# Performance work log

Measured on AMD Instinct MI355X. Metric: run time of the kernel, lower is better.

The kernel has to match this reference:

```python
import jax, jax.numpy as jnp
import numpy as np

N_NODES = 50000
N_EDGES = 1250000
D_FEAT = 64
UNITS = 64


def setup_inputs() -> dict:
    key = jax.random.key(0)
    k1, k2, k3, k4, k5 = jax.random.split(key, 5)
    src = jax.random.normal(k1, (N_NODES, D_FEAT), dtype=jnp.float32)
    edge = jax.random.randint(k2, (N_EDGES,), 0, N_EDGES, dtype=jnp.int32)  # unused by call()
    dst = jax.random.normal(k3, (N_EDGES, D_FEAT), dtype=jnp.float32)
    segment_ids = jnp.sort(
        jax.random.randint(k4, (N_EDGES, 1), 0, N_NODES, dtype=jnp.int32), axis=0
    )
    W = jax.random.normal(k5, (D_FEAT, UNITS), dtype=jnp.float32) * 0.05
    b = jnp.zeros((UNITS,), dtype=jnp.float32)
    return {"src": src, "edge": edge, "dst": dst, "segment_ids": segment_ids, "W": W, "b": b}


def reference(src, edge, dst, segment_ids, W, b):
    # h_i = Dense( segment_mean(dst, ids) + src )
    ids = jnp.squeeze(segment_ids, axis=-1)
    n = src.shape[0]
    sums = jax.ops.segment_sum(dst, ids, num_segments=n, indices_are_sorted=True)  # [N, D]
    counts = jax.ops.segment_sum(
        jnp.ones((ids.shape[0],), dtype=dst.dtype), ids, num_segments=n, indices_are_sorted=True
    )
    # tf.math.segment_mean outputs 0 for empty segments -> guard divide
    mean = sums / jnp.maximum(counts, 1.0)[:, None]  # [N, D]
    x = mean + src  # self-loop residual
    return x @ W + b  # linear activation (activation=None)
```

## Files before the change

### kernel.cpp

```cpp
#include <hip/hip_runtime.h>

constexpr int D = 64;

__global__ void seg_bounds(const int* __restrict__ ids, int* __restrict__ offs,
                           int n_nodes, int n_edges) {
    const int e = blockIdx.x * blockDim.x + threadIdx.x;
    if (e >= n_edges) return;
    const int cur  = ids[e];
    const int prev = (e == 0) ? -1 : ids[e - 1];
    for (int n = prev + 1; n <= cur; ++n) offs[n] = e;
    if (e == n_edges - 1) {
        for (int n = cur + 1; n <= n_nodes; ++n) offs[n] = n_edges;
    }
}

template <bool USE_OFFS>
__global__ __launch_bounds__(256, 8) void gcn_fused(
    const float* __restrict__ src,
    const float* __restrict__ dst,
    const int*   __restrict__ ids,
    const int*   __restrict__ offs,
    const float* __restrict__ Wm,
    const float* __restrict__ bv,
    float*       __restrict__ out,
    int n_nodes, int n_edges)
{
    __shared__ float sW[D][D];
    __shared__ float sx[4][D];

    const int tid = threadIdx.x;

    {
        const float4* W4  = (const float4*)Wm;
        float4*       sW4 = (float4*)&sW[0][0];
#pragma unroll
        for (int i = 0; i < 4; ++i) sW4[tid + 256 * i] = W4[tid + 256 * i];
    }
    __syncthreads();

    const int wave = tid >> 6;
    const int lane = tid & 63;
    const int node = blockIdx.x * 4 + wave;
    if (node >= n_nodes) return;

    int start_, end_;
    if (USE_OFFS) {
        start_ = offs[node];
        end_   = offs[node + 1];
    } else {
        const int key = node + (lane >> 5);
        int lo = 0, hi = n_edges;
        while (lo < hi) {
            const int mid = (lo + hi) >> 1;
            if (ids[mid] < key) lo = mid + 1; else hi = mid;
        }
        start_ = __shfl(lo, 0);
        end_   = __shfl(lo, 32);
    }
    const int cnt = end_ - start_;

    const int g = lane >> 4;
    const int f = lane & 15;

    float4 s4 = make_float4(0.f, 0.f, 0.f, 0.f);
    if (lane < 16) s4 = *((const float4*)(src + (size_t)node * D) + f);

    const float4* dst4 = (const float4*)dst;
    float4 a = make_float4(0.f, 0.f, 0.f, 0.f);

    const int nb   = (cnt + 3) >> 2;
    const int nb4  = (nb + 3) & ~3;
    const int last = end_ - 1;

#pragma unroll 1
    for (int b = 0; b < nb4; b += 4) {
#pragma unroll
        for (int u = 0; u < 4; ++u) {
            const int r  = start_ + g + 4 * (b + u);
            const int rc = min(r, last);
            const float4 v = dst4[rc * (D / 4) + f];
            const bool  m = (r < end_);
            a.x += m ? v.x : 0.0f;
            a.y += m ? v.y : 0.0f;
            a.z += m ? v.z : 0.0f;
            a.w += m ? v.w : 0.0f;
        }
    }

    a.x += __shfl_xor(a.x, 16); a.y += __shfl_xor(a.y, 16);
    a.z += __shfl_xor(a.z, 16); a.w += __shfl_xor(a.w, 16);
    a.x += __shfl_xor(a.x, 32); a.y += __shfl_xor(a.y, 32);
    a.z += __shfl_xor(a.z, 32); a.w += __shfl_xor(a.w, 32);

    if (lane < 16) {
        const float inv = 1.0f / fmaxf((float)cnt, 1.0f);
        float4 xv;
        xv.x = fmaf(a.x, inv, s4.x);
        xv.y = fmaf(a.y, inv, s4.y);
        xv.z = fmaf(a.z, inv, s4.z);
        xv.w = fmaf(a.w, inv, s4.w);
        *((float4*)&sx[wave][0] + f) = xv;
    }

    float acc = bv[lane];
#pragma unroll
    for (int k = 0; k < D; k += 4) {
        const float4 xk = *(const float4*)&sx[wave][k];
        acc = fmaf(xk.x, sW[k + 0][lane], acc);
        acc = fmaf(xk.y, sW[k + 1][lane], acc);
        acc = fmaf(xk.z, sW[k + 2][lane], acc);
        acc = fmaf(xk.w, sW[k + 3][lane], acc);
    }
    out[(size_t)node * D + lane] = acc;
}

extern "C" void kernel_launch(void* const* d_in, const int* in_sizes, int n_in,
                              void* d_out, int out_size, void* d_ws, size_t ws_size,
                              hipStream_t stream) {
    const float* src = (const float*)d_in[0];
    const float* dst = (const float*)d_in[2];
    const int*   ids = (const int*)d_in[3];
    const float* Wm  = (const float*)d_in[4];
    const float* bv  = (const float*)d_in[5];
    float* out = (float*)d_out;

    const int n_nodes = in_sizes[0] / D;
    const int n_edges = in_sizes[3];

    const int nblocks = (n_nodes + 3) / 4;

    if (ws_size >= (size_t)(n_nodes + 1) * sizeof(int)) {
        int* offs = (int*)d_ws;
        seg_bounds<<<(n_edges + 255) / 256, 256, 0, stream>>>(ids, offs, n_nodes, n_edges);
        gcn_fused<true><<<nblocks, 256, 0, stream>>>(src, dst, ids, offs, Wm, bv, out,
                                                     n_nodes, n_edges);
    } else {
        gcn_fused<false><<<nblocks, 256, 0, stream>>>(src, dst, ids, nullptr, Wm, bv, out,
                                                      n_nodes, n_edges);
    }
}
```

Before: 72.46 us.

## Drop shared-memory W staging, vectorize seg_bounds, and deepen gather unroll

Removes the per-block copy of the 16KB weight matrix into LDS and the barrier that follows, so the matvec reads W directly from global memory, where it should stay cache-resident. seg_bounds now handles four edges per thread using an int4 load. The edge-gather loop is unrolled to 8 rows per iteration for more memory-level parallelism, and the launch-bounds occupancy hint drops from 8 to 6. In exchange the matvec issues global/L1 loads instead of LDS reads, and the int4 load in seg_bounds assumes n_edges is a multiple of 4 (it reads out of bounds otherwise).

New measurement: 83.16 us. 1.15x slower.

```diff
diff --git a/kernel.cpp b/kernel.cpp
--- a/kernel.cpp
+++ b/kernel.cpp
@@ -4,18 +4,26 @@
 
 __global__ void seg_bounds(const int* __restrict__ ids, int* __restrict__ offs,
                            int n_nodes, int n_edges) {
-    const int e = blockIdx.x * blockDim.x + threadIdx.x;
-    if (e >= n_edges) return;
-    const int cur  = ids[e];
-    const int prev = (e == 0) ? -1 : ids[e - 1];
-    for (int n = prev + 1; n <= cur; ++n) offs[n] = e;
-    if (e == n_edges - 1) {
-        for (int n = cur + 1; n <= n_nodes; ++n) offs[n] = n_edges;
+    const int t  = blockIdx.x * blockDim.x + threadIdx.x;
+    const int e0 = t * 4;
+    if (e0 >= n_edges) return;
+    const int4 c4   = *(const int4*)(ids + e0);
+    const int  prev = (e0 == 0) ? -1 : ids[e0 - 1];
+    const int  cur[4] = {c4.x, c4.y, c4.z, c4.w};
+    int p = prev;
+#pragma unroll
+    for (int u = 0; u < 4; ++u) {
+        const int e = e0 + u;
+        for (int n = p + 1; n <= cur[u]; ++n) offs[n] = e;
+        p = cur[u];
+    }
+    if (e0 + 4 >= n_edges) {
+        for (int n = p + 1; n <= n_nodes; ++n) offs[n] = n_edges;
     }
 }
 
 template <bool USE_OFFS>
-__global__ __launch_bounds__(256, 8) void gcn_fused(
+__global__ __launch_bounds__(256, 6) void gcn_fused(
     const float* __restrict__ src,
     const float* __restrict__ dst,
     const int*   __restrict__ ids,
@@ -25,19 +33,9 @@
     float*       __restrict__ out,
     int n_nodes, int n_edges)
 {
-    __shared__ float sW[D][D];
     __shared__ float sx[4][D];
 
-    const int tid = threadIdx.x;
-
-    {
-        const float4* W4  = (const float4*)Wm;
-        float4*       sW4 = (float4*)&sW[0][0];
-#pragma unroll
-        for (int i = 0; i < 4; ++i) sW4[tid + 256 * i] = W4[tid + 256 * i];
-    }
-    __syncthreads();
-
+    const int tid  = threadIdx.x;
     const int wave = tid >> 6;
     const int lane = tid & 63;
     const int node = blockIdx.x * 4 + wave;
@@ -69,13 +67,13 @@
     float4 a = make_float4(0.f, 0.f, 0.f, 0.f);
 
     const int nb   = (cnt + 3) >> 2;
-    const int nb4  = (nb + 3) & ~3;
+    const int nb8  = (nb + 7) & ~7;
     const int last = end_ - 1;
 
 #pragma unroll 1
-    for (int b = 0; b < nb4; b += 4) {
+    for (int b = 0; b < nb8; b += 8) {
 #pragma unroll
-        for (int u = 0; u < 4; ++u) {
+        for (int u = 0; u < 8; ++u) {
             const int r  = start_ + g + 4 * (b + u);
             const int rc = min(r, last);
             const float4 v = dst4[rc * (D / 4) + f];
@@ -103,13 +101,13 @@
     }
 
     float acc = bv[lane];
-#pragma unroll
+#pragma unroll 4
     for (int k = 0; k < D; k += 4) {
         const float4 xk = *(const float4*)&sx[wave][k];
-        acc = fmaf(xk.x, sW[k + 0][lane], acc);
-        acc = fmaf(xk.y, sW[k + 1][lane], acc);
-        acc = fmaf(xk.z, sW[k + 2][lane], acc);
-        acc = fmaf(xk.w, sW[k + 3][lane], acc);
+        acc = fmaf(xk.x, Wm[(k + 0) * D + lane], acc);
+        acc = fmaf(xk.y, Wm[(k + 1) * D + lane], acc);
+        acc = fmaf(xk.z, Wm[(k + 2) * D + lane], acc);
+        acc = fmaf(xk.w, Wm[(k + 3) * D + lane], acc);
     }
     out[(size_t)node * D + lane] = acc;
 }
@@ -131,7 +129,8 @@
 
     if (ws_size >= (size_t)(n_nodes + 1) * sizeof(int)) {
         int* offs = (int*)d_ws;
-        seg_bounds<<<(n_edges + 255) / 256, 256, 0, stream>>>(ids, offs, n_nodes, n_edges);
+        const int t4 = (n_edges + 3) / 4;
+        seg_bounds<<<(t4 + 255) / 256, 256, 0, stream>>>(ids, offs, n_nodes, n_edges);
         gcn_fused<true><<<nblocks, 256, 0, stream>>>(src, dst, ids, offs, Wm, bv, out,
                                                      n_nodes, n_edges);
     } else {
```
